# Kernel tuning notes

Measured on AMD Instinct MI355X. Metric: run time of the kernel, lower is better.

## Reference

```python
import jax, jax.numpy as jnp
import numpy as np

DIM = 128
CODEBOOK_SCALE = 16384
N_TOKENS = 16384


def setup_inputs() -> dict:
    key = jax.random.key(0)
    k1, k2 = jax.random.split(key)
    x = jax.random.normal(k1, (N_TOKENS, DIM), dtype=jnp.float32)
    codebook = jax.random.normal(k2, (CODEBOOK_SCALE, DIM), dtype=jnp.float32)
    return {"x": x, "codebook": codebook}


def reference(x, codebook):
    # scores: [N, codebook_scale] = x @ codebook.T
    scores = jnp.einsum("nd,cd->nc", x, codebook)
    indices = jnp.argmax(scores, axis=-1)  # [N] int
    loss = jnp.zeros((), dtype=jnp.float32)  # original returns constant 0.0 loss
    return (indices, loss)
```

## Files before the change

kernel.cpp:

```cpp
#include <hip/hip_runtime.h>
#include <hip/hip_bf16.h>

#define NT 16384
#define ND 128
#define NC 16384
#define NSPLIT 8
#define MARGIN 0.4f
#define TILE_BYTES 16384
#define NTILES 32

typedef __bf16 bf16x8 __attribute__((ext_vector_type(8)));
typedef unsigned short u16x8 __attribute__((ext_vector_type(8)));
typedef float f32x4 __attribute__((ext_vector_type(4)));

static __device__ __forceinline__ unsigned short f2bf(float f) {
    unsigned u = __float_as_uint(f);
    return (unsigned short)((u + 0x7FFFu + ((u >> 16) & 1u)) >> 16);
}
static __device__ __forceinline__ float bf2f(unsigned short u) {
    return __uint_as_float(((unsigned)u) << 16);
}
static __device__ __forceinline__ bf16x8 u2b(u16x8 u) {
    return __builtin_bit_cast(bf16x8, u);
}
static __device__ __forceinline__ void gl2lds(const void* g, void* l) {
    __builtin_amdgcn_global_load_lds(
        (const __attribute__((address_space(1))) unsigned int*)g,
        (__attribute__((address_space(3))) unsigned int*)l, 16, 0, 0);
}

__global__ __launch_bounds__(512) void lfq_convert_cb(
    const float4* __restrict__ cb4, unsigned short* __restrict__ cbs)
{
    const unsigned i = blockIdx.x * 512 + threadIdx.x;
    float4 v = cb4[i];
    const unsigned c    = i >> 5;
    const unsigned d0   = (i & 31u) << 2;
    const unsigned tile = c >> 6, r = c & 63u;
    const unsigned pos  = ((d0 >> 3) + r) & 15u;
    const unsigned base = tile * 8192u + r * 128u + pos * 8u + (d0 & 7u);
    ushort4 h;
    h.x = f2bf(v.x);
    h.y = f2bf(v.y);
    h.z = f2bf(v.z);
    h.w = f2bf(v.w);
    *(ushort4*)(cbs + base) = h;
}

static __device__ __forceinline__ float exact_dot(
    const float4* __restrict__ xr4, const float* __restrict__ cf, int cidx)
{
    const float4* cr = (const float4*)(cf + (size_t)cidx * ND);
    float a0 = 0.f, a1 = 0.f, a2 = 0.f, a3 = 0.f;
#pragma unroll
    for (int i = 0; i < 32; i += 4) {
        float4 x0 = xr4[i+0], x1 = xr4[i+1], x2 = xr4[i+2], x3 = xr4[i+3];
        float4 c0 = cr[i+0],  c1 = cr[i+1],  c2 = cr[i+2],  c3 = cr[i+3];
        a0 += x0.x*c0.x + x0.y*c0.y + x0.z*c0.z + x0.w*c0.w;
        a1 += x1.x*c1.x + x1.y*c1.y + x1.z*c1.z + x1.w*c1.w;
        a2 += x2.x*c2.x + x2.y*c2.y + x2.z*c2.z + x2.w*c2.w;
        a3 += x3.x*c3.x + x3.y*c3.y + x3.z*c3.z + x3.w*c3.w;
    }
    return (a0 + a1) + (a2 + a3);
}

static __device__ __forceinline__ void mfma16(
    const bf16x8 ah[4][4], bf16x8 q0, bf16x8 q1, bf16x8 q2, bf16x8 q3,
    f32x4& a0, f32x4& a1, f32x4& a2, f32x4& a3)
{
    a0 = __builtin_amdgcn_mfma_f32_16x16x32_bf16(ah[0][0], q0, a0, 0,0,0);
    a1 = __builtin_amdgcn_mfma_f32_16x16x32_bf16(ah[1][0], q0, a1, 0,0,0);
    a2 = __builtin_amdgcn_mfma_f32_16x16x32_bf16(ah[2][0], q0, a2, 0,0,0);
    a3 = __builtin_amdgcn_mfma_f32_16x16x32_bf16(ah[3][0], q0, a3, 0,0,0);
    a0 = __builtin_amdgcn_mfma_f32_16x16x32_bf16(ah[0][1], q1, a0, 0,0,0);
    a1 = __builtin_amdgcn_mfma_f32_16x16x32_bf16(ah[1][1], q1, a1, 0,0,0);
    a2 = __builtin_amdgcn_mfma_f32_16x16x32_bf16(ah[2][1], q1, a2, 0,0,0);
    a3 = __builtin_amdgcn_mfma_f32_16x16x32_bf16(ah[3][1], q1, a3, 0,0,0);
    a0 = __builtin_amdgcn_mfma_f32_16x16x32_bf16(ah[0][2], q2, a0, 0,0,0);
    a1 = __builtin_amdgcn_mfma_f32_16x16x32_bf16(ah[1][2], q2, a1, 0,0,0);
    a2 = __builtin_amdgcn_mfma_f32_16x16x32_bf16(ah[2][2], q2, a2, 0,0,0);
    a3 = __builtin_amdgcn_mfma_f32_16x16x32_bf16(ah[3][2], q2, a3, 0,0,0);
    a0 = __builtin_amdgcn_mfma_f32_16x16x32_bf16(ah[0][3], q3, a0, 0,0,0);
    a1 = __builtin_amdgcn_mfma_f32_16x16x32_bf16(ah[1][3], q3, a1, 0,0,0);
    a2 = __builtin_amdgcn_mfma_f32_16x16x32_bf16(ah[2][3], q3, a2, 0,0,0);
    a3 = __builtin_amdgcn_mfma_f32_16x16x32_bf16(ah[3][3], q3, a3, 0,0,0);
}

static __device__ __forceinline__ void top2_upd(
    const f32x4& a, float* b1r, float* b2r, unsigned pk)
{
#pragma unroll
    for (int r4 = 0; r4 < 4; ++r4) {
        float p = __uint_as_float((__float_as_uint(a[r4]) & 0xFFFFFF80u) | pk);
        b2r[r4] = __builtin_amdgcn_fmed3f(p, b1r[r4], b2r[r4]);
        b1r[r4] = fmaxf(p, b1r[r4]);
    }
}

__global__ __launch_bounds__(256, 2) void lfq_stage1(
    const float* __restrict__ xf, const unsigned short* __restrict__ cbs,
    float* __restrict__ sb1, float* __restrict__ sb2,
    int* __restrict__ si1, int* __restrict__ si2)
{
    const int split = blockIdx.x & 7;
    const int tb    = blockIdx.x >> 3;
    const int t0    = tb * 256;
    const int tid   = threadIdx.x;
    const int w     = tid >> 6;
    const int lane  = tid & 63;
    const int n     = lane & 15;
    const int quad  = lane >> 4;

    __shared__ __attribute__((aligned(16))) unsigned char lds[2 * TILE_BYTES];

    bf16x8 ah[4][4];
#pragma unroll
    for (int tt = 0; tt < 4; ++tt) {
        const float* xr = xf + (size_t)(t0 + w * 64 + tt * 16 + n) * ND + quad * 8;
#pragma unroll
        for (int kk = 0; kk < 4; ++kk) {
            float4 v0 = *(const float4*)(xr + kk * 32);
            float4 v1 = *(const float4*)(xr + kk * 32 + 4);
            u16x8 hu;
            hu[0] = f2bf(v0.x);
            hu[1] = f2bf(v0.y);
            hu[2] = f2bf(v0.z);
            hu[3] = f2bf(v0.w);
            hu[4] = f2bf(v1.x);
            hu[5] = f2bf(v1.y);
            hu[6] = f2bf(v1.z);
            hu[7] = f2bf(v1.w);
            ah[tt][kk] = u2b(hu);
        }
    }

    float b1[4][4], b2[4][4];
#pragma unroll
    for (int tt = 0; tt < 4; ++tt)
#pragma unroll
        for (int r = 0; r < 4; ++r) { b1[tt][r] = -3.0e38f; b2[tt][r] = -3.0e38f; }

    const unsigned char* gtiles =
        (const unsigned char*)cbs + (size_t)(split * NTILES) * TILE_BYTES;
    const unsigned sgo  = (unsigned)(tid * 16);
    const unsigned ldso = (unsigned)(w * 1024);

    const unsigned bb0 = (unsigned)n * 256u + ((((unsigned)(quad + n     )) & 15u) << 4);
    const unsigned bb1 = (unsigned)n * 256u + ((((unsigned)(quad + n +  4)) & 15u) << 4);
    const unsigned bb2 = (unsigned)n * 256u + ((((unsigned)(quad + n +  8)) & 15u) << 4);
    const unsigned bb3 = (unsigned)n * 256u + ((((unsigned)(quad + n + 12)) & 15u) << 4);

#define RDQ(Q0, Q1, Q2, Q3, SOFF)                      \
    Q0 = *(const bf16x8*)&lds[(SOFF) + bb0];           \
    Q1 = *(const bf16x8*)&lds[(SOFF) + bb1];           \
    Q2 = *(const bf16x8*)&lds[(SOFF) + bb2];           \
    Q3 = *(const bf16x8*)&lds[(SOFF) + bb3];

#pragma unroll
    for (int rd = 0; rd < 4; ++rd)
        gl2lds(gtiles + rd * 4096 + sgo, &lds[rd * 4096 + ldso]);
    __syncthreads();

    const f32x4 z4 = {0.f, 0.f, 0.f, 0.f};
    for (int t = 0; t < NTILES; ++t) {
        const unsigned bufo = (unsigned)(t & 1) * TILE_BYTES;
        if (t < NTILES - 1) {
            const unsigned char* g = gtiles + (size_t)(t + 1) * TILE_BYTES;
            const unsigned nbo = (unsigned)((t + 1) & 1) * TILE_BYTES;
#pragma unroll
            for (int rd = 0; rd < 4; ++rd)
                gl2lds(g + rd * 4096 + sgo, &lds[nbo + rd * 4096 + ldso]);
        }
        f32x4 a0, a1, a2, a3;
        bf16x8 qa0, qa1, qa2, qa3, qb0, qb1, qb2, qb3;
        RDQ(qa0, qa1, qa2, qa3, bufo)
        RDQ(qb0, qb1, qb2, qb3, bufo + 4096u)
        a0 = z4; a1 = z4; a2 = z4; a3 = z4;
        mfma16(ah, qa0, qa1, qa2, qa3, a0, a1, a2, a3);
        {
            const unsigned pk = (unsigned)(127 - (t * 4 + 0));
            top2_upd(a0, b1[0], b2[0], pk);
            top2_upd(a1, b1[1], b2[1], pk);
            top2_upd(a2, b1[2], b2[2], pk);
            top2_upd(a3, b1[3], b2[3], pk);
        }
        RDQ(qa0, qa1, qa2, qa3, bufo + 8192u)
        a0 = z4; a1 = z4; a2 = z4; a3 = z4;
        mfma16(ah, qb0, qb1, qb2, qb3, a0, a1, a2, a3);
        {
            const unsigned pk = (unsigned)(127 - (t * 4 + 1));
            top2_upd(a0, b1[0], b2[0], pk);
            top2_upd(a1, b1[1], b2[1], pk);
            top2_upd(a2, b1[2], b2[2], pk);
            top2_upd(a3, b1[3], b2[3], pk);
        }
        RDQ(qb0, qb1, qb2, qb3, bufo + 12288u)
        a0 = z4; a1 = z4; a2 = z4; a3 = z4;
        mfma16(ah, qa0, qa1, qa2, qa3, a0, a1, a2, a3);
        {
            const unsigned pk = (unsigned)(127 - (t * 4 + 2));
            top2_upd(a0, b1[0], b2[0], pk);
            top2_upd(a1, b1[1], b2[1], pk);
            top2_upd(a2, b1[2], b2[2], pk);
            top2_upd(a3, b1[3], b2[3], pk);
        }
        a0 = z4; a1 = z4; a2 = z4; a3 = z4;
        mfma16(ah, qb0, qb1, qb2, qb3, a0, a1, a2, a3);
        {
            const unsigned pk = (unsigned)(127 - (t * 4 + 3));
            top2_upd(a0, b1[0], b2[0], pk);
            top2_upd(a1, b1[1], b2[1], pk);
            top2_upd(a2, b1[2], b2[2], pk);
            top2_upd(a3, b1[3], b2[3], pk);
        }
        __syncthreads();
    }
#undef RDQ

    const int cb_base = split * (NC / NSPLIT);
    float v1[4][4], v2[4][4];
    int   c1[4][4], c2[4][4];
#pragma unroll
    for (int tt = 0; tt < 4; ++tt)
#pragma unroll
        for (int r = 0; r < 4; ++r) {
            int j1 = 127 - (int)(__float_as_uint(b1[tt][r]) & 127u);
            int j2 = 127 - (int)(__float_as_uint(b2[tt][r]) & 127u);
            v1[tt][r] = b1[tt][r]; c1[tt][r] = cb_base + j1 * 16 + n;
            v2[tt][r] = b2[tt][r]; c2[tt][r] = cb_base + j2 * 16 + n;
        }

#pragma unroll
    for (int tt = 0; tt < 4; ++tt)
#pragma unroll
        for (int r = 0; r < 4; ++r) {
#pragma unroll
            for (int off = 1; off < 16; off <<= 1) {
                float ob1 = __shfl_xor(v1[tt][r], off, 64);
                int   oi1 = __shfl_xor(c1[tt][r], off, 64);
                float ob2 = __shfl_xor(v2[tt][r], off, 64);
                int   oi2 = __shfl_xor(c2[tt][r], off, 64);
                bool gt = (ob1 > v1[tt][r]) ||
                          (ob1 == v1[tt][r] && oi1 < c1[tt][r]);
                float ls = gt ? v1[tt][r] : ob1;
                int   li = gt ? c1[tt][r] : oi1;
                float ws_ = gt ? ob2 : v2[tt][r];
                int   wi = gt ? oi2 : c2[tt][r];
                bool s2 = (ls > ws_) || (ls == ws_ && li < wi);
                v2[tt][r] = s2 ? ls : ws_;
                c2[tt][r] = s2 ? li : wi;
                v1[tt][r] = gt ? ob1 : v1[tt][r];
                c1[tt][r] = gt ? oi1 : c1[tt][r];
            }
        }

    if (n == 0) {
#pragma unroll
        for (int tt = 0; tt < 4; ++tt)
#pragma unroll
            for (int r = 0; r < 4; ++r) {
                const int token = t0 + w * 64 + tt * 16 + quad * 4 + r;
                const size_t o = (size_t)split * NT + token;
                sb1[o] = v1[tt][r]; si1[o] = c1[tt][r];
                sb2[o] = v2[tt][r]; si2[o] = c2[tt][r];
            }
    }
}

__global__ __launch_bounds__(256) void lfq_combine(
    const float* __restrict__ sb1, const float* __restrict__ sb2,
    const int* __restrict__ si1, const int* __restrict__ si2,
    const float* __restrict__ xf, const float* __restrict__ cf,
    float* __restrict__ out, int out_size)
{
    const int t = blockIdx.x * 256 + threadIdx.x;

    float v[16]; int id[16];
#pragma unroll
    for (int s = 0; s < NSPLIT; ++s) {
        const size_t o = (size_t)s * NT + t;
        v[2*s]   = sb1[o]; id[2*s]   = si1[o];
        v[2*s+1] = sb2[o]; id[2*s+1] = si2[o];
    }
    float A1 = v[0]; int I1 = id[0];
#pragma unroll
    for (int k = 1; k < 16; ++k)
        if (v[k] > A1 || (v[k] == A1 && id[k] < I1)) { A1 = v[k]; I1 = id[k]; }

    int cnt = 0;
#pragma unroll
    for (int k = 0; k < 16; ++k) cnt += (v[k] >= A1 - MARGIN) ? 1 : 0;

    int bi = I1;
    if (cnt > 1) {
        float4 xr4[32];
        const float4* xrow = (const float4*)(xf + (size_t)t * ND);
#pragma unroll
        for (int i = 0; i < 32; ++i) xr4[i] = xrow[i];
        float bs = -__builtin_inff(); bool have = false; bi = 0;
#pragma unroll
        for (int k = 0; k < 16; ++k) {
            if (v[k] >= A1 - MARGIN) {
                float s = exact_dot(xr4, cf, id[k]);
                if (!have || s > bs || (s == bs && id[k] < bi)) { bs = s; bi = id[k]; have = true; }
            }
        }
    }
    out[t] = (float)bi;
    if (t == 0 && out_size > NT) out[NT] = 0.0f;
}

__global__ __launch_bounds__(512) void lfq_fp32_argmax(
    const float* __restrict__ xf, const float* __restrict__ cf,
    float* __restrict__ out, int out_size)
{
    const int tid = threadIdx.x;
    const int w   = tid >> 6;
    const int tok = tid & 63;
    const int t0  = blockIdx.x * 64;
    __shared__ float s_sc[8][64];
    __shared__ int   s_ix[8][64];

    float4 xr[32];
    const float4* xrow = (const float4*)(xf + (size_t)(t0 + tok) * ND);
#pragma unroll
    for (int i = 0; i < 32; ++i) xr[i] = xrow[i];

    float bs = -__builtin_inff();
    int   bi = 0;
    const int c_begin = w * (NC / 8);
    for (int c = c_begin; c < c_begin + NC / 8; ++c) {
        float s = exact_dot(xr, cf, c);
        if (s > bs) { bs = s; bi = c; }
    }
    s_sc[w][tok] = bs; s_ix[w][tok] = bi;
    __syncthreads();
    if (tid < 64) {
        float bsf = s_sc[0][tid]; int bif = s_ix[0][tid];
#pragma unroll
        for (int ww = 1; ww < 8; ++ww) {
            float s2 = s_sc[ww][tid]; int ii = s_ix[ww][tid];
            if (s2 > bsf || (s2 == bsf && ii < bif)) { bsf = s2; bif = ii; }
        }
        out[t0 + tid] = (float)bif;
    }
    if (blockIdx.x == 0 && tid == 0 && out_size > NT) out[NT] = 0.0f;
}

extern "C" void kernel_launch(void* const* d_in, const int* in_sizes, int n_in,
                              void* d_out, int out_size, void* d_ws, size_t ws_size,
                              hipStream_t stream) {
    const float* x  = (const float*)d_in[0];
    const float* cb = (const float*)d_in[1];
    float* out = (float*)d_out;

    const size_t NCE = (size_t)NC * ND;
    const size_t NEED = NCE * 2 + (size_t)NT * NSPLIT * 4 * 4;
    if (ws_size >= NEED) {
        char* ws = (char*)d_ws;
        unsigned short* cbs = (unsigned short*)ws;
        char* sp = ws + NCE * 2;
        float* sb1 = (float*)sp;
        float* sb2 = (float*)(sp + (size_t)NT * NSPLIT * 4);
        int*   si1 = (int*)  (sp + (size_t)NT * NSPLIT * 8);
        int*   si2 = (int*)  (sp + (size_t)NT * NSPLIT * 12);

        lfq_convert_cb<<<dim3(1024), dim3(512), 0, stream>>>(
            (const float4*)cb, cbs);
        lfq_stage1<<<dim3((NT / 256) * NSPLIT), dim3(256), 0, stream>>>(
            x, cbs, sb1, sb2, si1, si2);
        lfq_combine<<<dim3(64), dim3(256), 0, stream>>>(
            sb1, sb2, si1, si2, x, cb, out, out_size);
    } else {
        lfq_fp32_argmax<<<dim3(NT / 64), dim3(512), 0, stream>>>(x, cb, out, out_size);
    }
}
```

Baseline: 185.3 us.

## Halve stage1 token tile for more blocks and parallelize combine across lanes

Stage1 now handles 128 tokens per block instead of 256, doubling the grid to 1024 blocks and raising launch bounds to 4 blocks per SM. Each block therefore reloads the same codebook tiles for half as many tokens, which doubles codebook traffic through LDS in exchange for occupancy. The combine kernel now spreads each token over 8 lanes, one per split, and reduces with shuffles. The exact fp32 rescoring is also split across those lanes, so the combine grid grows from 64 blocks to many more.

```diff
diff --git a/kernel.cpp b/kernel.cpp
--- a/kernel.cpp
+++ b/kernel.cpp
@@ -64,26 +64,37 @@
     return (a0 + a1) + (a2 + a3);
 }
 
-static __device__ __forceinline__ void mfma16(
-    const bf16x8 ah[4][4], bf16x8 q0, bf16x8 q1, bf16x8 q2, bf16x8 q3,
-    f32x4& a0, f32x4& a1, f32x4& a2, f32x4& a3)
+static __device__ __forceinline__ float exact_dot_g(
+    const float* __restrict__ xf, const float* __restrict__ cf,
+    int token, int cidx)
+{
+    const float4* xr = (const float4*)(xf + (size_t)token * ND);
+    const float4* cr = (const float4*)(cf + (size_t)cidx * ND);
+    float a0 = 0.f, a1 = 0.f, a2 = 0.f, a3 = 0.f;
+#pragma unroll
+    for (int i = 0; i < 32; i += 4) {
+        float4 x0 = xr[i+0], x1 = xr[i+1], x2 = xr[i+2], x3 = xr[i+3];
+        float4 c0 = cr[i+0], c1 = cr[i+1], c2 = cr[i+2], c3 = cr[i+3];
+        a0 += x0.x*c0.x + x0.y*c0.y + x0.z*c0.z + x0.w*c0.w;
+        a1 += x1.x*c1.x + x1.y*c1.y + x1.z*c1.z + x1.w*c1.w;
+        a2 += x2.x*c2.x + x2.y*c2.y + x2.z*c2.z + x2.w*c2.w;
+        a3 += x3.x*c3.x + x3.y*c3.y + x3.z*c3.z + x3.w*c3.w;
+    }
+    return (a0 + a1) + (a2 + a3);
+}
+
+static __device__ __forceinline__ void mfma8(
+    const bf16x8 ah[2][4], bf16x8 q0, bf16x8 q1, bf16x8 q2, bf16x8 q3,
+    f32x4& a0, f32x4& a1)
 {
     a0 = __builtin_amdgcn_mfma_f32_16x16x32_bf16(ah[0][0], q0, a0, 0,0,0);
     a1 = __builtin_amdgcn_mfma_f32_16x16x32_bf16(ah[1][0], q0, a1, 0,0,0);
-    a2 = __builtin_amdgcn_mfma_f32_16x16x32_bf16(ah[2][0], q0, a2, 0,0,0);
-    a3 = __builtin_amdgcn_mfma_f32_16x16x32_bf16(ah[3][0], q0, a3, 0,0,0);
     a0 = __builtin_amdgcn_mfma_f32_16x16x32_bf16(ah[0][1], q1, a0, 0,0,0);
     a1 = __builtin_amdgcn_mfma_f32_16x16x32_bf16(ah[1][1], q1, a1, 0,0,0);
-    a2 = __builtin_amdgcn_mfma_f32_16x16x32_bf16(ah[2][1], q1, a2, 0,0,0);
-    a3 = __builtin_amdgcn_mfma_f32_16x16x32_bf16(ah[3][1], q1, a3, 0,0,0);
     a0 = __builtin_amdgcn_mfma_f32_16x16x32_bf16(ah[0][2], q2, a0, 0,0,0);
     a1 = __builtin_amdgcn_mfma_f32_16x16x32_bf16(ah[1][2], q2, a1, 0,0,0);
-    a2 = __builtin_amdgcn_mfma_f32_16x16x32_bf16(ah[2][2], q2, a2, 0,0,0);
-    a3 = __builtin_amdgcn_mfma_f32_16x16x32_bf16(ah[3][2], q2, a3, 0,0,0);
     a0 = __builtin_amdgcn_mfma_f32_16x16x32_bf16(ah[0][3], q3, a0, 0,0,0);
     a1 = __builtin_amdgcn_mfma_f32_16x16x32_bf16(ah[1][3], q3, a1, 0,0,0);
-    a2 = __builtin_amdgcn_mfma_f32_16x16x32_bf16(ah[2][3], q3, a2, 0,0,0);
-    a3 = __builtin_amdgcn_mfma_f32_16x16x32_bf16(ah[3][3], q3, a3, 0,0,0);
 }
 
 static __device__ __forceinline__ void top2_upd(
@@ -97,14 +108,14 @@
     }
 }
 
-__global__ __launch_bounds__(256, 2) void lfq_stage1(
+__global__ __launch_bounds__(256, 4) void lfq_stage1(
     const float* __restrict__ xf, const unsigned short* __restrict__ cbs,
     float* __restrict__ sb1, float* __restrict__ sb2,
     int* __restrict__ si1, int* __restrict__ si2)
 {
     const int split = blockIdx.x & 7;
     const int tb    = blockIdx.x >> 3;
-    const int t0    = tb * 256;
+    const int t0    = tb * 128;
     const int tid   = threadIdx.x;
     const int w     = tid >> 6;
     const int lane  = tid & 63;
@@ -113,10 +124,10 @@
 
     __shared__ __attribute__((aligned(16))) unsigned char lds[2 * TILE_BYTES];
 
-    bf16x8 ah[4][4];
-#pragma unroll
-    for (int tt = 0; tt < 4; ++tt) {
-        const float* xr = xf + (size_t)(t0 + w * 64 + tt * 16 + n) * ND + quad * 8;
+    bf16x8 ah[2][4];
+#pragma unroll
+    for (int tt = 0; tt < 2; ++tt) {
+        const float* xr = xf + (size_t)(t0 + w * 32 + tt * 16 + n) * ND + quad * 8;
 #pragma unroll
         for (int kk = 0; kk < 4; ++kk) {
             float4 v0 = *(const float4*)(xr + kk * 32);
@@ -134,9 +145,9 @@
         }
     }
 
-    float b1[4][4], b2[4][4];
-#pragma unroll
-    for (int tt = 0; tt < 4; ++tt)
+    float b1[2][4], b2[2][4];
+#pragma unroll
+    for (int tt = 0; tt < 2; ++tt)
 #pragma unroll
         for (int r = 0; r < 4; ++r) { b1[tt][r] = -3.0e38f; b2[tt][r] = -3.0e38f; }
 
@@ -149,12 +160,6 @@
     const unsigned bb1 = (unsigned)n * 256u + ((((unsigned)(quad + n +  4)) & 15u) << 4);
     const unsigned bb2 = (unsigned)n * 256u + ((((unsigned)(quad + n +  8)) & 15u) << 4);
     const unsigned bb3 = (unsigned)n * 256u + ((((unsigned)(quad + n + 12)) & 15u) << 4);
-
-#define RDQ(Q0, Q1, Q2, Q3, SOFF)                      \
-    Q0 = *(const bf16x8*)&lds[(SOFF) + bb0];           \
-    Q1 = *(const bf16x8*)&lds[(SOFF) + bb1];           \
-    Q2 = *(const bf16x8*)&lds[(SOFF) + bb2];           \
-    Q3 = *(const bf16x8*)&lds[(SOFF) + bb3];
 
 #pragma unroll
     for (int rd = 0; rd < 4; ++rd)
@@ -171,57 +176,67 @@
             for (int rd = 0; rd < 4; ++rd)
                 gl2lds(g + rd * 4096 + sgo, &lds[nbo + rd * 4096 + ldso]);
         }
-        f32x4 a0, a1, a2, a3;
-        bf16x8 qa0, qa1, qa2, qa3, qb0, qb1, qb2, qb3;
-        RDQ(qa0, qa1, qa2, qa3, bufo)
-        RDQ(qb0, qb1, qb2, qb3, bufo + 4096u)
-        a0 = z4; a1 = z4; a2 = z4; a3 = z4;
-        mfma16(ah, qa0, qa1, qa2, qa3, a0, a1, a2, a3);
+        f32x4 aA0, aA1, aB0, aB1;
+        {
+            bf16x8 q0 = *(const bf16x8*)&lds[bufo + bb0];
+            bf16x8 q1 = *(const bf16x8*)&lds[bufo + bb1];
+            bf16x8 q2 = *(const bf16x8*)&lds[bufo + bb2];
+            bf16x8 q3 = *(const bf16x8*)&lds[bufo + bb3];
+            aA0 = z4; aA1 = z4;
+            mfma8(ah, q0, q1, q2, q3, aA0, aA1);
+        }
+        {
+            bf16x8 q0 = *(const bf16x8*)&lds[bufo + 4096u + bb0];
+            bf16x8 q1 = *(const bf16x8*)&lds[bufo + 4096u + bb1];
+            bf16x8 q2 = *(const bf16x8*)&lds[bufo + 4096u + bb2];
+            bf16x8 q3 = *(const bf16x8*)&lds[bufo + 4096u + bb3];
+            aB0 = z4; aB1 = z4;
+            mfma8(ah, q0, q1, q2, q3, aB0, aB1);
+        }
         {
             const unsigned pk = (unsigned)(127 - (t * 4 + 0));
-            top2_upd(a0, b1[0], b2[0], pk);
-            top2_upd(a1, b1[1], b2[1], pk);
-            top2_upd(a2, b1[2], b2[2], pk);
-            top2_upd(a3, b1[3], b2[3], pk);
-        }
-        RDQ(qa0, qa1, qa2, qa3, bufo + 8192u)
-        a0 = z4; a1 = z4; a2 = z4; a3 = z4;
-        mfma16(ah, qb0, qb1, qb2, qb3, a0, a1, a2, a3);
+            top2_upd(aA0, b1[0], b2[0], pk);
+            top2_upd(aA1, b1[1], b2[1], pk);
+        }
+        {
+            bf16x8 q0 = *(const bf16x8*)&lds[bufo + 8192u + bb0];
+            bf16x8 q1 = *(const bf16x8*)&lds[bufo + 8192u + bb1];
+            bf16x8 q2 = *(const bf16x8*)&lds[bufo + 8192u + bb2];
+            bf16x8 q3 = *(const bf16x8*)&lds[bufo + 8192u + bb3];
+            aA0 = z4; aA1 = z4;
+            mfma8(ah, q0, q1, q2, q3, aA0, aA1);
+        }
         {
             const unsigned pk = (unsigned)(127 - (t * 4 + 1));
-            top2_upd(a0, b1[0], b2[0], pk);
-            top2_upd(a1, b1[1], b2[1], pk);
-            top2_upd(a2, b1[2], b2[2], pk);
-            top2_upd(a3, b1[3], b2[3], pk);
-        }
-        RDQ(qb0, qb1, qb2, qb3, bufo + 12288u)
-        a0 = z4; a1 = z4; a2 = z4; a3 = z4;
-        mfma16(ah, qa0, qa1, qa2, qa3, a0, a1, a2, a3);
+            top2_upd(aB0, b1[0], b2[0], pk);
+            top2_upd(aB1, b1[1], b2[1], pk);
+        }
+        {
+            bf16x8 q0 = *(const bf16x8*)&lds[bufo + 12288u + bb0];
+            bf16x8 q1 = *(const bf16x8*)&lds[bufo + 12288u + bb1];
+            bf16x8 q2 = *(const bf16x8*)&lds[bufo + 12288u + bb2];
+            bf16x8 q3 = *(const bf16x8*)&lds[bufo + 12288u + bb3];
+            aB0 = z4; aB1 = z4;
+            mfma8(ah, q0, q1, q2, q3, aB0, aB1);
+        }
         {
             const unsigned pk = (unsigned)(127 - (t * 4 + 2));
-            top2_upd(a0, b1[0], b2[0], pk);
-            top2_upd(a1, b1[1], b2[1], pk);
-            top2_upd(a2, b1[2], b2[2], pk);
-            top2_upd(a3, b1[3], b2[3], pk);
-        }
-        a0 = z4; a1 = z4; a2 = z4; a3 = z4;
-        mfma16(ah, qb0, qb1, qb2, qb3, a0, a1, a2, a3);
+            top2_upd(aA0, b1[0], b2[0], pk);
+            top2_upd(aA1, b1[1], b2[1], pk);
+        }
         {
             const unsigned pk = (unsigned)(127 - (t * 4 + 3));
-            top2_upd(a0, b1[0], b2[0], pk);
-            top2_upd(a1, b1[1], b2[1], pk);
-            top2_upd(a2, b1[2], b2[2], pk);
-            top2_upd(a3, b1[3], b2[3], pk);
+            top2_upd(aB0, b1[0], b2[0], pk);
+            top2_upd(aB1, b1[1], b2[1], pk);
         }
         __syncthreads();
     }
-#undef RDQ
 
     const int cb_base = split * (NC / NSPLIT);
-    float v1[4][4], v2[4][4];
-    int   c1[4][4], c2[4][4];
-#pragma unroll
-    for (int tt = 0; tt < 4; ++tt)
+    float v1[2][4], v2[2][4];
+    int   c1[2][4], c2[2][4];
+#pragma unroll
+    for (int tt = 0; tt < 2; ++tt)
 #pragma unroll
         for (int r = 0; r < 4; ++r) {
             int j1 = 127 - (int)(__float_as_uint(b1[tt][r]) & 127u);
@@ -231,7 +246,7 @@
         }
 
 #pragma unroll
-    for (int tt = 0; tt < 4; ++tt)
+    for (int tt = 0; tt < 2; ++tt)
 #pragma unroll
         for (int r = 0; r < 4; ++r) {
 #pragma unroll
@@ -256,10 +271,10 @@
 
     if (n == 0) {
 #pragma unroll
-        for (int tt = 0; tt < 4; ++tt)
+        for (int tt = 0; tt < 2; ++tt)
 #pragma unroll
             for (int r = 0; r < 4; ++r) {
-                const int token = t0 + w * 64 + tt * 16 + quad * 4 + r;
+                const int token = t0 + w * 32 + tt * 16 + quad * 4 + r;
                 const size_t o = (size_t)split * NT + token;
                 sb1[o] = v1[tt][r]; si1[o] = c1[tt][r];
                 sb2[o] = v2[tt][r]; si2[o] = c2[tt][r];
@@ -273,41 +288,53 @@
     const float* __restrict__ xf, const float* __restrict__ cf,
     float* __restrict__ out, int out_size)
 {
-    const int t = blockIdx.x * 256 + threadIdx.x;
-
-    float v[16]; int id[16];
-#pragma unroll
-    for (int s = 0; s < NSPLIT; ++s) {
-        const size_t o = (size_t)s * NT + t;
-        v[2*s]   = sb1[o]; id[2*s]   = si1[o];
-        v[2*s+1] = sb2[o]; id[2*s+1] = si2[o];
-    }
-    float A1 = v[0]; int I1 = id[0];
-#pragma unroll
-    for (int k = 1; k < 16; ++k)
-        if (v[k] > A1 || (v[k] == A1 && id[k] < I1)) { A1 = v[k]; I1 = id[k]; }
-
-    int cnt = 0;
-#pragma unroll
-    for (int k = 0; k < 16; ++k) cnt += (v[k] >= A1 - MARGIN) ? 1 : 0;
+    const int lane = threadIdx.x & 63;
+    const int wv   = threadIdx.x >> 6;
+    const int g    = lane >> 3;
+    const int cl   = lane & 7;
+    const int t    = (blockIdx.x * 4 + wv) * 8 + g;
+
+    const size_t o = (size_t)cl * NT + t;
+    const float va = sb1[o]; const int ia = si1[o];
+    const float vb = sb2[o]; const int ib = si2[o];
+
+    bool lgt = (vb > va) || (vb == va && ib < ia);
+    float m  = lgt ? vb : va;
+    int   mi = lgt ? ib : ia;
+#pragma unroll
+    for (int off = 1; off < 8; off <<= 1) {
+        float om = __shfl_xor(m, off, 64);
+        int   oi = __shfl_xor(mi, off, 64);
+        if (om > m || (om == m && oi < mi)) { m = om; mi = oi; }
+    }
+    const float A1 = m;
+    const int   I1 = mi;
+
+    const bool ba = (va >= A1 - MARGIN);
+    const bool bb_ = (vb >= A1 - MARGIN);
+    int cnt = (ba ? 1 : 0) + (bb_ ? 1 : 0);
+#pragma unroll
+    for (int off = 1; off < 8; off <<= 1)
+        cnt += __shfl_xor(cnt, off, 64);
 
     int bi = I1;
     if (cnt > 1) {
-        float4 xr4[32];
-        const float4* xrow = (const float4*)(xf + (size_t)t * ND);
-#pragma unroll
-        for (int i = 0; i < 32; ++i) xr4[i] = xrow[i];
-        float bs = -__builtin_inff(); bool have = false; bi = 0;
-#pragma unroll
-        for (int k = 0; k < 16; ++k) {
-            if (v[k] >= A1 - MARGIN) {
-                float s = exact_dot(xr4, cf, id[k]);
-                if (!have || s > bs || (s == bs && id[k] < bi)) { bs = s; bi = id[k]; have = true; }
-            }
-        }
-    }
-    out[t] = (float)bi;
-    if (t == 0 && out_size > NT) out[NT] = 0.0f;
+        float sa = -__builtin_inff(), sb_ = -__builtin_inff();
+        if (ba)  sa  = exact_dot_g(xf, cf, t, ia);
+        if (bb_) sb_ = exact_dot_g(xf, cf, t, ib);
+        bool g2 = (sb_ > sa) || (sb_ == sa && ib < ia);
+        float bs = g2 ? sb_ : sa;
+        int  bid = g2 ? ib : ia;
+#pragma unroll
+        for (int off = 1; off < 8; off <<= 1) {
+            float os = __shfl_xor(bs, off, 64);
+            int   oi = __shfl_xor(bid, off, 64);
+            if (os > bs || (os == bs && oi < bid)) { bs = os; bid = oi; }
+        }
+        bi = bid;
+    }
+    if (cl == 0) out[t] = (float)bi;
+    if (blockIdx.x == 0 && threadIdx.x == 0 && out_size > NT) out[NT] = 0.0f;
 }
 
 __global__ __launch_bounds__(512) void lfq_fp32_argmax(
@@ -367,9 +394,9 @@
 
         lfq_convert_cb<<<dim3(1024), dim3(512), 0, stream>>>(
             (const float4*)cb, cbs);
-        lfq_stage1<<<dim3((NT / 256) * NSPLIT), dim3(256), 0, stream>>>(
+        lfq_stage1<<<dim3((NT / 128) * NSPLIT), dim3(256), 0, stream>>>(
             x, cbs, sb1, sb2, si1, si2);
-        lfq_combine<<<dim3(64), dim3(256), 0, stream>>>(
+        lfq_combine<<<dim3(NT / 32), dim3(256), 0, stream>>>(
             sb1, sb2, si1, si2, x, cb, out, out_size);
     } else {
         lfq_fp32_argmax<<<dim3(NT / 64), dim3(512), 0, stream>>>(x, cb, out, out_size);
```

Result: faster. 162.3 us (-12.4%).
